# Optimization experiments

Hardware: AMD Instinct MI355X
Metric: run time of the kernel (lower is better)

## Reference

```python
import jax, jax.numpy as jnp
import numpy as np

D_MODEL, NHEAD, INT_DIM = 1024, 16, 4096
HEAD_DIM = D_MODEL // NHEAD
EPS = 1e-5


def _layernorm(x, gamma, beta):
    mu = jnp.mean(x, axis=-1, keepdims=True)
    var = jnp.var(x, axis=-1, keepdims=True)
    return (x - mu) * jax.lax.rsqrt(var + EPS) * gamma + beta


def setup_inputs() -> dict:
    key = jax.random.key(0)
    ks = jax.random.split(key, 16)
    B, T = 2, 2048
    s = 0.02
    inp = {
        'x': jax.random.normal(ks[0], (B, T, D_MODEL), dtype=jnp.float32),
        'Wq': jax.random.normal(ks[1], (D_MODEL, D_MODEL), dtype=jnp.float32) * s,
        'bq': jnp.zeros((D_MODEL,), jnp.float32),
        'Wk': jax.random.normal(ks[2], (D_MODEL, D_MODEL), dtype=jnp.float32) * s,
        'bk': jnp.zeros((D_MODEL,), jnp.float32),
        'Wv': jax.random.normal(ks[3], (D_MODEL, D_MODEL), dtype=jnp.float32) * s,
        'bv': jnp.zeros((D_MODEL,), jnp.float32),
        'Wo': jax.random.normal(ks[4], (D_MODEL, D_MODEL), dtype=jnp.float32) * s,
        'bo': jnp.zeros((D_MODEL,), jnp.float32),
        'ln1_g': jnp.ones((D_MODEL,), jnp.float32),
        'ln1_b': jnp.zeros((D_MODEL,), jnp.float32),
        'ln2_g': jnp.ones((D_MODEL,), jnp.float32),
        'ln2_b': jnp.zeros((D_MODEL,), jnp.float32),
        'W1': jax.random.normal(ks[5], (D_MODEL, INT_DIM), dtype=jnp.float32) * s,
        'b1': jnp.zeros((INT_DIM,), jnp.float32),
        'W2': jax.random.normal(ks[6], (INT_DIM, D_MODEL), dtype=jnp.float32) * s,
        'b2': jnp.zeros((D_MODEL,), jnp.float32),
    }
    return inp


def reference(x, Wq, bq, Wk, bk, Wv, bv, Wo, bo, ln1_g, ln1_b, ln2_g, ln2_b, W1, b1, W2, b2):
    B, T, D = x.shape
    # projections
    q = (x @ Wq + bq).reshape(B, T, NHEAD, HEAD_DIM).transpose(0, 2, 1, 3)
    k = (x @ Wk + bk).reshape(B, T, NHEAD, HEAD_DIM).transpose(0, 2, 1, 3)
    v = (x @ Wv + bv).reshape(B, T, NHEAD, HEAD_DIM).transpose(0, 2, 1, 3)
    # attention: [B,H,T,T] scores, softmax over keys
    scores = jnp.einsum('bhqd,bhkd->bhqk', q, k) / jnp.sqrt(jnp.float32(HEAD_DIM))
    attn = jax.nn.softmax(scores, axis=-1)
    out = jnp.einsum('bhqk,bhkd->bhqd', attn, v)
    out = out.transpose(0, 2, 1, 3).reshape(B, T, D)
    attn_output = out @ Wo + bo
    # residual + layernorm 1
    h = _layernorm(x + attn_output, ln1_g, ln1_b)
    # FFN
    ff = jax.nn.relu(h @ W1 + b1) @ W2 + b2
    # residual + layernorm 2
    return _layernorm(h + ff, ln2_g, ln2_b)
```

## Files before the change

### kernel.cpp

```cpp
#include <hip/hip_runtime.h>
#include <cstdint>

#define DEVI __device__ __forceinline__

typedef float f32x4 __attribute__((ext_vector_type(4)));
typedef __bf16 bf16x8 __attribute__((ext_vector_type(8)));
typedef unsigned int u32x4v __attribute__((ext_vector_type(4)));
typedef unsigned short u16;
typedef unsigned int u32;
typedef unsigned long long u64;

#define LOG2E 1.44269504088896f
#define QSCALE (0.125f * LOG2E)

DEVI u16 bf16bits(float f) {
    u32 u = __builtin_bit_cast(u32, f);
    u32 r = u + 0x7fffu + ((u >> 16) & 1u);
    return (u16)(r >> 16);
}

DEVI u32 pack2bf(float a, float b) {
    u16 x = __builtin_bit_cast(u16, (__bf16)a);
    u16 y = __builtin_bit_cast(u16, (__bf16)b);
    return (u32)x | ((u32)y << 16);
}

DEVI void gload16(const void* g, const void* l) {
    __builtin_amdgcn_global_load_lds(
        (const __attribute__((address_space(1))) void*)(u64)(uintptr_t)g,
        (__attribute__((address_space(3))) void*)(u32)(uintptr_t)l,
        16, 0, 0);
}

__global__ __launch_bounds__(256)
void prep_kernel(const float* __restrict__ x, u16* __restrict__ xb,
                 const float* __restrict__ Wq, const float* __restrict__ Wk,
                 const float* __restrict__ Wv, const float* __restrict__ Wo,
                 u16* __restrict__ Wqt, u16* __restrict__ Wkt,
                 u16* __restrict__ Wvt, u16* __restrict__ Wot,
                 const float* __restrict__ W1, u16* __restrict__ W1t,
                 const float* __restrict__ W2, u16* __restrict__ W2t) {
    __shared__ float t[64][65];
    const int b = blockIdx.x;
    const int tid = threadIdx.x;
    if (b < 4096) {
        int i = b * 256 + tid;
        float4 v = ((const float4*)x)[i];
        u32 lo = pack2bf(v.x, v.y);
        u32 hi = pack2bf(v.z, v.w);
        ((uint2*)xb)[i] = make_uint2(lo, hi);
        return;
    }
    const float* src;
    u16* dst;
    int K_, N_, k0, n0;
    if (b < 5120) {
        int l = b - 4096;
        int z = l >> 8;
        l &= 255;
        src = z == 0 ? Wq : z == 1 ? Wk : z == 2 ? Wv : Wo;
        dst = z == 0 ? Wqt : z == 1 ? Wkt : z == 2 ? Wvt : Wot;
        K_ = 1024; N_ = 1024;
        k0 = (l & 15) * 64; n0 = (l >> 4) * 64;
    } else if (b < 6144) {
        int l = b - 5120;
        src = W1; dst = W1t; K_ = 1024; N_ = 4096;
        k0 = (l & 15) * 64; n0 = (l >> 4) * 64;
    } else {
        int l = b - 6144;
        src = W2; dst = W2t; K_ = 4096; N_ = 1024;
        k0 = (l & 63) * 64; n0 = (l >> 6) * 64;
    }
#pragma unroll
    for (int i = 0; i < 16; i++) {
        int idx = i * 256 + tid;
        int r = idx >> 6, c = idx & 63;
        t[r][c] = src[(u64)(k0 + r) * N_ + n0 + c];
    }
    __syncthreads();
#pragma unroll
    for (int i = 0; i < 16; i++) {
        int idx = i * 256 + tid;
        int r = idx >> 6, c = idx & 63;
        dst[(u64)(n0 + r) * K_ + k0 + c] = bf16bits(t[c][r]);
    }
}

enum { MODE_QK = 0, MODE_VT = 1, MODE_RESID = 2, MODE_RELU = 3 };

DEVI void gemm_core(const u16* __restrict__ A, const u16* __restrict__ Bt, int K_,
                    u16* ldsA, u16* ldsB, f32x4 (&acc)[4][4], int m0, int n0) {
    const int tid = threadIdx.x;
    const int lane = tid & 63;
    const int wid = tid >> 6;
    const int wr = wid >> 1, wc = wid & 1;
    const int l15 = lane & 15, l4 = lane >> 4;

    for (int kt = 0; kt < K_; kt += 64) {
        __syncthreads();
#pragma unroll
        for (int i = 0; i < 4; i++) {
            int s = i * 256 + tid;
            int row = s >> 3, c = s & 7;
            gload16(A + (u64)(m0 + row) * K_ + kt + ((c ^ (row & 7)) * 8),
                    (const char*)ldsA + s * 16);
        }
#pragma unroll
        for (int i = 0; i < 4; i++) {
            int s = i * 256 + tid;
            int row = s >> 3, c = s & 7;
            gload16(Bt + (u64)(n0 + row) * K_ + kt + ((c ^ (row & 7)) * 8),
                    (const char*)ldsB + s * 16);
        }
        __syncthreads();
#pragma unroll
        for (int ks = 0; ks < 2; ks++) {
            bf16x8 af[4], bfr[4];
#pragma unroll
            for (int mi = 0; mi < 4; mi++) {
                int row = wr * 64 + mi * 16 + l15;
                af[mi] = *(const bf16x8*)((const char*)ldsA + row * 128 +
                                          (((ks * 4 + l4) ^ (row & 7)) * 16));
            }
#pragma unroll
            for (int ni = 0; ni < 4; ni++) {
                int row = wc * 64 + ni * 16 + l15;
                bfr[ni] = *(const bf16x8*)((const char*)ldsB + row * 128 +
                                           (((ks * 4 + l4) ^ (row & 7)) * 16));
            }
            __builtin_amdgcn_s_setprio(1);
#pragma unroll
            for (int mi = 0; mi < 4; mi++)
#pragma unroll
                for (int ni = 0; ni < 4; ni++)
                    acc[mi][ni] = __builtin_amdgcn_mfma_f32_16x16x32_bf16(
                        af[mi], bfr[ni], acc[mi][ni], 0, 0, 0);
            __builtin_amdgcn_s_setprio(0);
        }
    }
}

template <int MODE>
DEVI void gemm_epilogue(f32x4 (&acc)[4][4], const float* __restrict__ bias,
                        const float* __restrict__ resid, void* __restrict__ outp,
                        int N_, int m0, int n0, float scale) {
    const int tid = threadIdx.x;
    const int lane = tid & 63;
    const int wid = tid >> 6;
    const int wr = wid >> 1, wc = wid & 1;
    const int l15 = lane & 15, l4 = lane >> 4;
#pragma unroll
    for (int mi = 0; mi < 4; mi++) {
#pragma unroll
        for (int ni = 0; ni < 4; ni++) {
            const int n = n0 + wc * 64 + ni * 16 + l15;
            const float bv = bias[n];
            const int mb = m0 + wr * 64 + mi * 16 + l4 * 4;
            if (MODE == MODE_VT) {
                const int b = mb >> 11, t = mb & 2047;
                const int hh = n >> 6, d = n & 63;
                u32 lo = pack2bf(acc[mi][ni][0] + bv, acc[mi][ni][1] + bv);
                u32 hi = pack2bf(acc[mi][ni][2] + bv, acc[mi][ni][3] + bv);
                u64 idx = ((u64)((b << 4) + hh) * 64 + d) * 2048 + t;
                *(uint2*)((u16*)outp + idx) = make_uint2(lo, hi);
            } else {
#pragma unroll
                for (int r = 0; r < 4; r++) {
                    const int m = mb + r;
                    const float v = acc[mi][ni][r] + bv;
                    if (MODE == MODE_QK) {
                        const int b = m >> 11, t = m & 2047;
                        const int hh = n >> 6, d = n & 63;
                        ((u16*)outp)[(((u64)((b << 4) + hh) * 2048 + t) << 6) + d] =
                            bf16bits(v * scale);
                    } else if (MODE == MODE_RESID) {
                        const u64 i2 = (u64)m * N_ + n;
                        ((float*)outp)[i2] = v + resid[i2];
                    } else {
                        ((u16*)outp)[(u64)m * N_ + n] = bf16bits(fmaxf(v, 0.f));
                    }
                }
            }
        }
    }
}

template <int MODE>
__global__ __launch_bounds__(256, 2)
void gemm_kernel(const u16* __restrict__ A, const u16* __restrict__ Bt,
                 const float* __restrict__ bias, const float* __restrict__ resid,
                 void* __restrict__ outp, int N_, int K_) {
    __shared__ u16 ldsA[128 * 64];
    __shared__ u16 ldsB[128 * 64];
    const int m0 = blockIdx.x * 128;
    const int n0 = blockIdx.y * 128;
    f32x4 acc[4][4];
#pragma unroll
    for (int i = 0; i < 4; i++)
#pragma unroll
        for (int j = 0; j < 4; j++) acc[i][j] = (f32x4){0.f, 0.f, 0.f, 0.f};
    gemm_core(A, Bt, K_, ldsA, ldsB, acc, m0, n0);
    gemm_epilogue<MODE>(acc, bias, resid, outp, N_, m0, n0, 1.f);
}

__global__ __launch_bounds__(256, 2)
void gemm_qkv_kernel(const u16* __restrict__ A,
                     const u16* __restrict__ Wq, const u16* __restrict__ Wk,
                     const u16* __restrict__ Wv,
                     const float* __restrict__ bq, const float* __restrict__ bk,
                     const float* __restrict__ bv,
                     u16* __restrict__ Qo, u16* __restrict__ Ko, u16* __restrict__ Vo) {
    __shared__ u16 ldsA[128 * 64];
    __shared__ u16 ldsB[128 * 64];
    const int z = blockIdx.z;
    const u16* Bt = z == 0 ? Wq : z == 1 ? Wk : Wv;
    const float* bias = z == 0 ? bq : z == 1 ? bk : bv;
    const int m0 = blockIdx.x * 128;
    const int n0 = blockIdx.y * 128;
    f32x4 acc[4][4];
#pragma unroll
    for (int i = 0; i < 4; i++)
#pragma unroll
        for (int j = 0; j < 4; j++) acc[i][j] = (f32x4){0.f, 0.f, 0.f, 0.f};
    gemm_core(A, Bt, 1024, ldsA, ldsB, acc, m0, n0);
    if (z == 2)
        gemm_epilogue<MODE_VT>(acc, bias, nullptr, Vo, 1024, m0, n0, 1.f);
    else
        gemm_epilogue<MODE_QK>(acc, bias, nullptr, z == 0 ? Qo : Ko, 1024, m0, n0,
                               z == 0 ? QSCALE : 1.f);
}

__global__ __launch_bounds__(256, 2)
void gemm_n64_kernel(const u16* __restrict__ A, const u16* __restrict__ Bt,
                     const float* __restrict__ bias, const float* __restrict__ resid,
                     float* __restrict__ outp, int K_) {
    __shared__ u16 ldsA[2][128 * 64];
    __shared__ u16 ldsB[2][64 * 64];
    const int tid = threadIdx.x;
    const int lane = tid & 63;
    const int wid = tid >> 6;
    const int m0 = blockIdx.x * 128;
    const int n0 = blockIdx.y * 64;
    const int l15 = lane & 15, l4 = lane >> 4;

    auto stage = [&](int buf, int kt) {
#pragma unroll
        for (int i = 0; i < 4; i++) {
            int s = i * 256 + tid;
            int row = s >> 3, c = s & 7;
            gload16(A + (u64)(m0 + row) * K_ + kt + ((c ^ (row & 7)) * 8),
                    (const char*)ldsA[buf] + s * 16);
        }
#pragma unroll
        for (int i = 0; i < 2; i++) {
            int s = i * 256 + tid;
            int row = s >> 3, c = s & 7;
            gload16(Bt + (u64)(n0 + row) * K_ + kt + ((c ^ (row & 7)) * 8),
                    (const char*)ldsB[buf] + s * 16);
        }
    };

    f32x4 acc[2][4];
#pragma unroll
    for (int i = 0; i < 2; i++)
#pragma unroll
        for (int j = 0; j < 4; j++) acc[i][j] = (f32x4){0.f, 0.f, 0.f, 0.f};

    stage(0, 0);
    const int nk = K_ >> 6;
    for (int t = 0; t < nk; t++) {
        const int cur = t & 1;
        asm volatile("s_waitcnt vmcnt(0)" ::: "memory");
        __builtin_amdgcn_s_barrier();
        if (t + 1 < nk) stage(cur ^ 1, (t + 1) * 64);
        const u16* A_ = ldsA[cur];
        const u16* B_ = ldsB[cur];
#pragma unroll
        for (int ks = 0; ks < 2; ks++) {
            bf16x8 af[2], bfr[4];
#pragma unroll
            for (int mi = 0; mi < 2; mi++) {
                int row = wid * 32 + mi * 16 + l15;
                af[mi] = *(const bf16x8*)((const char*)A_ + row * 128 +
                                          (((ks * 4 + l4) ^ (row & 7)) * 16));
            }
#pragma unroll
            for (int ni = 0; ni < 4; ni++) {
                int row = ni * 16 + l15;
                bfr[ni] = *(const bf16x8*)((const char*)B_ + row * 128 +
                                           (((ks * 4 + l4) ^ (row & 7)) * 16));
            }
            __builtin_amdgcn_s_setprio(1);
#pragma unroll
            for (int mi = 0; mi < 2; mi++)
#pragma unroll
                for (int ni = 0; ni < 4; ni++)
                    acc[mi][ni] = __builtin_amdgcn_mfma_f32_16x16x32_bf16(
                        af[mi], bfr[ni], acc[mi][ni], 0, 0, 0);
            __builtin_amdgcn_s_setprio(0);
        }
        __builtin_amdgcn_s_barrier();
    }

#pragma unroll
    for (int mi = 0; mi < 2; mi++) {
#pragma unroll
        for (int ni = 0; ni < 4; ni++) {
            const int n = n0 + ni * 16 + l15;
            const float bv = bias[n];
            const int mb = m0 + wid * 32 + mi * 16 + l4 * 4;
#pragma unroll
            for (int r = 0; r < 4; r++) {
                const u64 i2 = (u64)(mb + r) * 1024 + n;
                outp[i2] = acc[mi][ni][r] + bv + resid[i2];
            }
        }
    }
}

__global__ __launch_bounds__(256, 5)
void attn_kernel(const u16* __restrict__ Qg, const u16* __restrict__ Kg,
                 const u16* __restrict__ Vtg, u16* __restrict__ Og) {
    __shared__ u16 ldsK[2][64 * 64];
    __shared__ u16 ldsV[2][64 * 64];
    const int tid = threadIdx.x;
    const int lane = tid & 63;
    const int w = tid >> 6;
    const int l15 = lane & 15, l4 = lane >> 4;
    const int id = blockIdx.x;
    const int swz = (id & 7) * 128 + (id >> 3);
    const int bh = swz >> 5;
    const int qblk = swz & 31;
    const u64 kvbase = (u64)bh * 2048 * 64;
    const int qw0 = qblk * 64 + w * 16;

    auto stage = [&](int buf, int kt) {
#pragma unroll
        for (int i = 0; i < 2; i++) {
            int s = i * 256 + tid; int row = s >> 3, c = s & 7;
            gload16(Kg + kvbase + (u64)(kt + row) * 64 + ((c ^ (row & 7)) * 8),
                    (const char*)ldsK[buf] + s * 16);
        }
#pragma unroll
        for (int i = 0; i < 2; i++) {
            int s = i * 256 + tid; int row = s >> 3, c = s & 7;
            gload16(Vtg + kvbase + (u64)row * 2048 + kt + ((c ^ (row & 7)) * 8),
                    (const char*)ldsV[buf] + s * 16);
        }
    };

    stage(0, 0);

    bf16x8 aq[2];
#pragma unroll
    for (int ks = 0; ks < 2; ks++)
        aq[ks] = *(const bf16x8*)(Qg + kvbase + (u64)(qw0 + l15) * 64 + ks * 32 + l4 * 8);

    f32x4 acco[4];
#pragma unroll
    for (int i = 0; i < 4; i++) acco[i] = (f32x4){0.f, 0.f, 0.f, 0.f};
    float la0 = 0.f, la1 = 0.f;

    asm volatile("s_waitcnt vmcnt(0)" ::: "memory");
    __builtin_amdgcn_s_barrier();

    for (int t = 0; t < 32; t++) {
        const int cur = t & 1;
        if (t < 31) stage(cur ^ 1, (t + 1) * 64);
        const u16* K_ = ldsK[cur];
        const u16* V_ = ldsV[cur];

        f32x4 sf[4];
#pragma unroll
        for (int f = 0; f < 4; f++) sf[f] = (f32x4){0.f, 0.f, 0.f, 0.f};
#pragma unroll
        for (int ks = 0; ks < 2; ks++) {
            bf16x8 ak[4];
#pragma unroll
            for (int f = 0; f < 4; f++) {
                int row = f * 16 + l15;
                ak[f] = *(const bf16x8*)((const char*)K_ + row * 128 +
                                         (((ks * 4 + l4) ^ (row & 7)) * 16));
            }
            __builtin_amdgcn_s_setprio(1);
#pragma unroll
            for (int f = 0; f < 4; f++)
                sf[f] = __builtin_amdgcn_mfma_f32_16x16x32_bf16(ak[f], aq[ks], sf[f], 0, 0, 0);
            __builtin_amdgcn_s_setprio(0);
        }

        u32 A[4], B[4];
#pragma unroll
        for (int f = 0; f < 4; f++) {
            float p0 = exp2f(sf[f][0]);
            float p1 = exp2f(sf[f][1]);
            float p2 = exp2f(sf[f][2]);
            float p3 = exp2f(sf[f][3]);
            la0 += p0 + p2;
            la1 += p1 + p3;
            A[f] = pack2bf(p0, p1);
            B[f] = pack2bf(p2, p3);
        }
        asm volatile("v_permlane32_swap_b32 %0, %1" : "+v"(A[0]), "+v"(A[1]));
        asm volatile("v_permlane16_swap_b32 %0, %1" : "+v"(A[0]), "+v"(A[1]));
        asm volatile("v_permlane32_swap_b32 %0, %1" : "+v"(B[0]), "+v"(B[1]));
        asm volatile("v_permlane16_swap_b32 %0, %1" : "+v"(B[0]), "+v"(B[1]));
        asm volatile("v_permlane32_swap_b32 %0, %1" : "+v"(A[2]), "+v"(A[3]));
        asm volatile("v_permlane16_swap_b32 %0, %1" : "+v"(A[2]), "+v"(A[3]));
        asm volatile("v_permlane32_swap_b32 %0, %1" : "+v"(B[2]), "+v"(B[3]));
        asm volatile("v_permlane16_swap_b32 %0, %1" : "+v"(B[2]), "+v"(B[3]));

#pragma unroll
        for (int ks = 0; ks < 2; ks++) {
            u32x4v pw = {A[2 * ks], B[2 * ks], A[2 * ks + 1], B[2 * ks + 1]};
            bf16x8 pfrag = __builtin_bit_cast(bf16x8, pw);
            bf16x8 av[4];
#pragma unroll
            for (int nf = 0; nf < 4; nf++) {
                int row = nf * 16 + l15;
                av[nf] = *(const bf16x8*)((const char*)V_ + row * 128 +
                                          (((ks * 4 + l4) ^ (row & 7)) * 16));
            }
            __builtin_amdgcn_s_setprio(1);
#pragma unroll
            for (int nf = 0; nf < 4; nf++)
                acco[nf] = __builtin_amdgcn_mfma_f32_16x16x32_bf16(av[nf], pfrag, acco[nf], 0, 0, 0);
            __builtin_amdgcn_s_setprio(0);
        }

        asm volatile("s_waitcnt vmcnt(0)" ::: "memory");
        __builtin_amdgcn_s_barrier();
    }

    float lacc = la0 + la1;
    lacc += __shfl_xor(lacc, 16, 64);
    lacc += __shfl_xor(lacc, 32, 64);
    const float inv = 1.f / lacc;

    const int b = bh >> 4, h = bh & 15;
    const int tq = qw0 + l15;
#pragma unroll
    for (int nf = 0; nf < 4; nf++) {
        const int d = nf * 16 + l4 * 4;
        u32 lo = pack2bf(acco[nf][0] * inv, acco[nf][1] * inv);
        u32 hi = pack2bf(acco[nf][2] * inv, acco[nf][3] * inv);
        *(uint2*)(Og + ((u64)(b * 2048 + tq) << 10) + h * 64 + d) = make_uint2(lo, hi);
    }
}

template <bool WB16>
__global__ __launch_bounds__(256, 4)
void ln_kernel(const float* __restrict__ in, const float* __restrict__ gam,
               const float* __restrict__ bet, float* __restrict__ outf,
               u16* __restrict__ outb) {
    __shared__ float red[2][4];
    const int row = blockIdx.x;
    const int tid = threadIdx.x;
    float4 v = ((const float4*)(in + (u64)row * 1024))[tid];
    float s = v.x + v.y + v.z + v.w;
    float sq = v.x * v.x + v.y * v.y + v.z * v.z + v.w * v.w;
#pragma unroll
    for (int sh = 1; sh < 64; sh <<= 1) {
        s += __shfl_xor(s, sh, 64);
        sq += __shfl_xor(sq, sh, 64);
    }
    if ((tid & 63) == 0) { red[0][tid >> 6] = s; red[1][tid >> 6] = sq; }
    __syncthreads();
    s = red[0][0] + red[0][1] + red[0][2] + red[0][3];
    sq = red[1][0] + red[1][1] + red[1][2] + red[1][3];
    float mu = s * (1.f / 1024.f);
    float var = sq * (1.f / 1024.f) - mu * mu;
    float inv = rsqrtf(var + 1e-5f);
    float4 g = ((const float4*)gam)[tid];
    float4 bb = ((const float4*)bet)[tid];
    float4 o;
    o.x = (v.x - mu) * inv * g.x + bb.x;
    o.y = (v.y - mu) * inv * g.y + bb.y;
    o.z = (v.z - mu) * inv * g.z + bb.z;
    o.w = (v.w - mu) * inv * g.w + bb.w;
    ((float4*)(outf + (u64)row * 1024))[tid] = o;
    if (WB16) {
        u32 lo = pack2bf(o.x, o.y);
        u32 hi = pack2bf(o.z, o.w);
        ((uint2*)(outb + (u64)row * 1024))[tid] = make_uint2(lo, hi);
    }
}

extern "C" void kernel_launch(void* const* d_in, const int* in_sizes, int n_in,
                              void* d_out, int out_size, void* d_ws, size_t ws_size,
                              hipStream_t stream) {
    (void)in_sizes; (void)n_in; (void)out_size; (void)ws_size;
    const float* x  = (const float*)d_in[0];
    const float* Wq = (const float*)d_in[1];
    const float* bq = (const float*)d_in[2];
    const float* Wk = (const float*)d_in[3];
    const float* bk = (const float*)d_in[4];
    const float* Wv = (const float*)d_in[5];
    const float* bv = (const float*)d_in[6];
    const float* Wo = (const float*)d_in[7];
    const float* bo = (const float*)d_in[8];
    const float* g1 = (const float*)d_in[9];
    const float* be1 = (const float*)d_in[10];
    const float* g2 = (const float*)d_in[11];
    const float* be2 = (const float*)d_in[12];
    const float* W1 = (const float*)d_in[13];
    const float* b1 = (const float*)d_in[14];
    const float* W2 = (const float*)d_in[15];
    const float* b2 = (const float*)d_in[16];

    char* ws = (char*)d_ws;
    const u64 MB = 1024ull * 1024ull;
    u16* xb    = (u16*)(ws + 0);
    u16* Wqt   = (u16*)(ws + 8 * MB);
    u16* Wkt   = (u16*)(ws + 10 * MB);
    u16* Wvt   = (u16*)(ws + 12 * MB);
    u16* Wot   = (u16*)(ws + 14 * MB);
    u16* W1t   = (u16*)(ws + 16 * MB);
    u16* W2t   = (u16*)(ws + 24 * MB);
    u16* Qb    = (u16*)(ws + 32 * MB);
    u16* Kb    = (u16*)(ws + 40 * MB);
    u16* Vtb   = (u16*)(ws + 48 * MB);
    u16* Ob    = (u16*)(ws + 56 * MB);
    float* pre1 = (float*)(ws + 64 * MB);
    float* hf  = (float*)(ws + 80 * MB);
    u16* hb    = (u16*)(ws + 96 * MB);
    u16* ffb   = (u16*)(ws + 104 * MB);
    float* pre2 = (float*)(ws + 64 * MB);

    prep_kernel<<<7168, 256, 0, stream>>>(x, xb, Wq, Wk, Wv, Wo,
                                          Wqt, Wkt, Wvt, Wot, W1, W1t, W2, W2t);

    gemm_qkv_kernel<<<dim3(32, 8, 3), 256, 0, stream>>>(xb, Wqt, Wkt, Wvt,
                                                        bq, bk, bv, Qb, Kb, Vtb);

    attn_kernel<<<1024, 256, 0, stream>>>(Qb, Kb, Vtb, Ob);

    gemm_n64_kernel<<<dim3(32, 16), 256, 0, stream>>>(Ob, Wot, bo, x, pre1, 1024);
    ln_kernel<true><<<4096, 256, 0, stream>>>(pre1, g1, be1, hf, hb);
    gemm_kernel<MODE_RELU><<<dim3(32, 32), 256, 0, stream>>>(hb, W1t, b1, nullptr, ffb, 4096, 1024);
    gemm_n64_kernel<<<dim3(32, 16), 256, 0, stream>>>(ffb, W2t, b2, hf, pre2, 4096);
    ln_kernel<false><<<4096, 256, 0, stream>>>(pre2, g2, be2, (float*)d_out, nullptr);
}
```

Baseline: 214.5 us.

## Double-buffer LDS in main GEMMs and hoist load address computation

The main GEMM core (QKV and generic GEMMs) previously loaded each K-tile into a single LDS buffer with two syncthreads per iteration, so global loads did not overlap compute. It now uses two LDS buffers, prefetching the next tile while the current one is computed, with one waitcnt and barrier per tile and a loop unrolled by two. Global load pointers are also precomputed once and advanced incrementally in the GEMMs and attention, which removes per-iteration index arithmetic. The cost is doubled LDS use per block (64KB), which may lower occupancy under launch_bounds(256,2).

After: 213.4 us. About the same (-0.5%).

```diff
diff --git a/kernel.cpp b/kernel.cpp
--- a/kernel.cpp
+++ b/kernel.cpp
@@ -31,6 +31,10 @@
         (__attribute__((address_space(3))) void*)(u32)(uintptr_t)l,
         16, 0, 0);
 }
+
+#define VMCNT0_BARRIER()                                   \
+    asm volatile("s_waitcnt vmcnt(0)" ::: "memory");       \
+    __builtin_amdgcn_s_barrier()
 
 __global__ __launch_bounds__(256)
 void prep_kernel(const float* __restrict__ x, u16* __restrict__ xb,
@@ -46,9 +50,7 @@
     if (b < 4096) {
         int i = b * 256 + tid;
         float4 v = ((const float4*)x)[i];
-        u32 lo = pack2bf(v.x, v.y);
-        u32 hi = pack2bf(v.z, v.w);
-        ((uint2*)xb)[i] = make_uint2(lo, hi);
+        ((uint2*)xb)[i] = make_uint2(pack2bf(v.x, v.y), pack2bf(v.z, v.w));
         return;
     }
     const float* src;
@@ -89,43 +91,51 @@
 enum { MODE_QK = 0, MODE_VT = 1, MODE_RESID = 2, MODE_RELU = 3 };
 
 DEVI void gemm_core(const u16* __restrict__ A, const u16* __restrict__ Bt, int K_,
-                    u16* ldsA, u16* ldsB, f32x4 (&acc)[4][4], int m0, int n0) {
+                    u16 (*ldsA)[128 * 64], u16 (*ldsB)[128 * 64],
+                    f32x4 (&acc)[4][4], int m0, int n0) {
     const int tid = threadIdx.x;
     const int lane = tid & 63;
     const int wid = tid >> 6;
     const int wr = wid >> 1, wc = wid & 1;
     const int l15 = lane & 15, l4 = lane >> 4;
-
-    for (int kt = 0; kt < K_; kt += 64) {
-        __syncthreads();
+    const int srow = tid >> 3;
+    const int sc = (tid & 7) ^ (srow & 7);
+
+    const u16* ap[4];
+    const u16* bp[4];
+#pragma unroll
+    for (int i = 0; i < 4; i++) {
+        ap[i] = A + (u64)(m0 + i * 32 + srow) * K_ + sc * 8;
+        bp[i] = Bt + (u64)(n0 + i * 32 + srow) * K_ + sc * 8;
+    }
+
+    auto stage = [&](int buf) {
 #pragma unroll
         for (int i = 0; i < 4; i++) {
-            int s = i * 256 + tid;
-            int row = s >> 3, c = s & 7;
-            gload16(A + (u64)(m0 + row) * K_ + kt + ((c ^ (row & 7)) * 8),
-                    (const char*)ldsA + s * 16);
+            gload16(ap[i], (const char*)ldsA[buf] + (i * 256 + tid) * 16);
+            ap[i] += 64;
         }
 #pragma unroll
         for (int i = 0; i < 4; i++) {
-            int s = i * 256 + tid;
-            int row = s >> 3, c = s & 7;
-            gload16(Bt + (u64)(n0 + row) * K_ + kt + ((c ^ (row & 7)) * 8),
-                    (const char*)ldsB + s * 16);
-        }
-        __syncthreads();
+            gload16(bp[i], (const char*)ldsB[buf] + (i * 256 + tid) * 16);
+            bp[i] += 64;
+        }
+    };
+
+    auto compute = [&](const u16* A_, const u16* B_) {
 #pragma unroll
         for (int ks = 0; ks < 2; ks++) {
             bf16x8 af[4], bfr[4];
 #pragma unroll
             for (int mi = 0; mi < 4; mi++) {
                 int row = wr * 64 + mi * 16 + l15;
-                af[mi] = *(const bf16x8*)((const char*)ldsA + row * 128 +
+                af[mi] = *(const bf16x8*)((const char*)A_ + row * 128 +
                                           (((ks * 4 + l4) ^ (row & 7)) * 16));
             }
 #pragma unroll
             for (int ni = 0; ni < 4; ni++) {
                 int row = wc * 64 + ni * 16 + l15;
-                bfr[ni] = *(const bf16x8*)((const char*)ldsB + row * 128 +
+                bfr[ni] = *(const bf16x8*)((const char*)B_ + row * 128 +
                                            (((ks * 4 + l4) ^ (row & 7)) * 16));
             }
             __builtin_amdgcn_s_setprio(1);
@@ -137,6 +147,18 @@
                         af[mi], bfr[ni], acc[mi][ni], 0, 0, 0);
             __builtin_amdgcn_s_setprio(0);
         }
+    };
+
+    const int nk = K_ >> 6;
+    stage(0);
+    VMCNT0_BARRIER();
+    for (int t = 0; t < nk; t += 2) {
+        if (t + 1 < nk) stage(1);
+        compute(ldsA[0], ldsB[0]);
+        VMCNT0_BARRIER();
+        if (t + 2 < nk) stage(0);
+        compute(ldsA[1], ldsB[1]);
+        VMCNT0_BARRIER();
     }
 }
 
@@ -190,8 +212,8 @@
 void gemm_kernel(const u16* __restrict__ A, const u16* __restrict__ Bt,
                  const float* __restrict__ bias, const float* __restrict__ resid,
                  void* __restrict__ outp, int N_, int K_) {
-    __shared__ u16 ldsA[128 * 64];
-    __shared__ u16 ldsB[128 * 64];
+    __shared__ u16 ldsA[2][128 * 64];
+    __shared__ u16 ldsB[2][128 * 64];
     const int m0 = blockIdx.x * 128;
     const int n0 = blockIdx.y * 128;
     f32x4 acc[4][4];
@@ -210,8 +232,8 @@
                      const float* __restrict__ bq, const float* __restrict__ bk,
                      const float* __restrict__ bv,
                      u16* __restrict__ Qo, u16* __restrict__ Ko, u16* __restrict__ Vo) {
-    __shared__ u16 ldsA[128 * 64];
-    __shared__ u16 ldsB[128 * 64];
+    __shared__ u16 ldsA[2][128 * 64];
+    __shared__ u16 ldsB[2][128 * 64];
     const int z = blockIdx.z;
     const u16* Bt = z == 0 ? Wq : z == 1 ? Wk : Wv;
     const float* bias = z == 0 ? bq : z == 1 ? bk : bv;
@@ -242,21 +264,28 @@
     const int m0 = blockIdx.x * 128;
     const int n0 = blockIdx.y * 64;
     const int l15 = lane & 15, l4 = lane >> 4;
-
-    auto stage = [&](int buf, int kt) {
+    const int srow = tid >> 3;
+    const int sc = (tid & 7) ^ (srow & 7);
+
+    const u16* ap[4];
+    const u16* bp[2];
+#pragma unroll
+    for (int i = 0; i < 4; i++)
+        ap[i] = A + (u64)(m0 + i * 32 + srow) * K_ + sc * 8;
+#pragma unroll
+    for (int i = 0; i < 2; i++)
+        bp[i] = Bt + (u64)(n0 + i * 32 + srow) * K_ + sc * 8;
+
+    auto stage = [&](int buf) {
 #pragma unroll
         for (int i = 0; i < 4; i++) {
-            int s = i * 256 + tid;
-            int row = s >> 3, c = s & 7;
-            gload16(A + (u64)(m0 + row) * K_ + kt + ((c ^ (row & 7)) * 8),
-                    (const char*)ldsA[buf] + s * 16);
+            gload16(ap[i], (const char*)ldsA[buf] + (i * 256 + tid) * 16);
+            ap[i] += 64;
         }
 #pragma unroll
         for (int i = 0; i < 2; i++) {
-            int s = i * 256 + tid;
-            int row = s >> 3, c = s & 7;
-            gload16(Bt + (u64)(n0 + row) * K_ + kt + ((c ^ (row & 7)) * 8),
-                    (const char*)ldsB[buf] + s * 16);
+            gload16(bp[i], (const char*)ldsB[buf] + (i * 256 + tid) * 16);
+            bp[i] += 64;
         }
     };
 
@@ -266,15 +295,7 @@
 #pragma unroll
         for (int j = 0; j < 4; j++) acc[i][j] = (f32x4){0.f, 0.f, 0.f, 0.f};
 
-    stage(0, 0);
-    const int nk = K_ >> 6;
-    for (int t = 0; t < nk; t++) {
-        const int cur = t & 1;
-        asm volatile("s_waitcnt vmcnt(0)" ::: "memory");
-        __builtin_amdgcn_s_barrier();
-        if (t + 1 < nk) stage(cur ^ 1, (t + 1) * 64);
-        const u16* A_ = ldsA[cur];
-        const u16* B_ = ldsB[cur];
+    auto compute = [&](const u16* A_, const u16* B_) {
 #pragma unroll
         for (int ks = 0; ks < 2; ks++) {
             bf16x8 af[2], bfr[4];
@@ -299,7 +320,18 @@
                         af[mi], bfr[ni], acc[mi][ni], 0, 0, 0);
             __builtin_amdgcn_s_setprio(0);
         }
-        __builtin_amdgcn_s_barrier();
+    };
+
+    const int nk = K_ >> 6;
+    stage(0);
+    VMCNT0_BARRIER();
+    for (int t = 0; t < nk; t += 2) {
+        if (t + 1 < nk) stage(1);
+        compute(ldsA[0], ldsB[0]);
+        VMCNT0_BARRIER();
+        if (t + 2 < nk) stage(0);
+        compute(ldsA[1], ldsB[1]);
+        VMCNT0_BARRIER();
     }
 
 #pragma unroll
@@ -334,22 +366,22 @@
     const u64 kvbase = (u64)bh * 2048 * 64;
     const int qw0 = qblk * 64 + w * 16;
 
-    auto stage = [&](int buf, int kt) {
-#pragma unroll
-        for (int i = 0; i < 2; i++) {
-            int s = i * 256 + tid; int row = s >> 3, c = s & 7;
-            gload16(Kg + kvbase + (u64)(kt + row) * 64 + ((c ^ (row & 7)) * 8),
-                    (const char*)ldsK[buf] + s * 16);
-        }
-#pragma unroll
-        for (int i = 0; i < 2; i++) {
-            int s = i * 256 + tid; int row = s >> 3, c = s & 7;
-            gload16(Vtg + kvbase + (u64)row * 2048 + kt + ((c ^ (row & 7)) * 8),
-                    (const char*)ldsV[buf] + s * 16);
-        }
+    const int srow = tid >> 3;
+    const int sc8 = ((tid & 7) ^ (srow & 7)) * 8;
+    const u16* kq0 = Kg + kvbase + (u64)srow * 64 + sc8;
+    const u16* kq1 = Kg + kvbase + (u64)(srow + 32) * 64 + sc8;
+    const u16* vq0 = Vtg + kvbase + (u64)srow * 2048 + sc8;
+    const u16* vq1 = Vtg + kvbase + (u64)(srow + 32) * 2048 + sc8;
+
+    auto stage = [&](int buf) {
+        gload16(kq0, (const char*)ldsK[buf] + tid * 16);
+        gload16(kq1, (const char*)ldsK[buf] + (256 + tid) * 16);
+        gload16(vq0, (const char*)ldsV[buf] + tid * 16);
+        gload16(vq1, (const char*)ldsV[buf] + (256 + tid) * 16);
+        kq0 += 4096; kq1 += 4096; vq0 += 64; vq1 += 64;
     };
 
-    stage(0, 0);
+    stage(0);
 
     bf16x8 aq[2];
 #pragma unroll
@@ -361,15 +393,7 @@
     for (int i = 0; i < 4; i++) acco[i] = (f32x4){0.f, 0.f, 0.f, 0.f};
     float la0 = 0.f, la1 = 0.f;
 
-    asm volatile("s_waitcnt vmcnt(0)" ::: "memory");
-    __builtin_amdgcn_s_barrier();
-
-    for (int t = 0; t < 32; t++) {
-        const int cur = t & 1;
-        if (t < 31) stage(cur ^ 1, (t + 1) * 64);
-        const u16* K_ = ldsK[cur];
-        const u16* V_ = ldsV[cur];
-
+    auto tile_body = [&](const u16* K_, const u16* V_) {
         f32x4 sf[4];
 #pragma unroll
         for (int f = 0; f < 4; f++) sf[f] = (f32x4){0.f, 0.f, 0.f, 0.f};
@@ -427,9 +451,17 @@
                 acco[nf] = __builtin_amdgcn_mfma_f32_16x16x32_bf16(av[nf], pfrag, acco[nf], 0, 0, 0);
             __builtin_amdgcn_s_setprio(0);
         }
-
-        asm volatile("s_waitcnt vmcnt(0)" ::: "memory");
-        __builtin_amdgcn_s_barrier();
+    };
+
+    VMCNT0_BARRIER();
+
+    for (int t = 0; t < 32; t += 2) {
+        if (t + 1 < 32) stage(1);
+        tile_body(ldsK[0], ldsV[0]);
+        VMCNT0_BARRIER();
+        if (t + 2 < 32) stage(0);
+        tile_body(ldsK[1], ldsV[1]);
+        VMCNT0_BARRIER();
     }
 
     float lacc = la0 + la1;
@@ -480,9 +512,7 @@
     o.w = (v.w - mu) * inv * g.w + bb.w;
     ((float4*)(outf + (u64)row * 1024))[tid] = o;
     if (WB16) {
-        u32 lo = pack2bf(o.x, o.y);
-        u32 hi = pack2bf(o.z, o.w);
-        ((uint2*)(outb + (u64)row * 1024))[tid] = make_uint2(lo, hi);
+        ((uint2*)(outb + (u64)row * 1024))[tid] = make_uint2(pack2bf(o.x, o.y), pack2bf(o.z, o.w));
     }
 }
 
```
